# Optimization experiments

Hardware: AMD Instinct MI355X
Metric: run time of the kernel (lower is better)

## Reference

```python
import jax, jax.numpy as jnp
import numpy as np

D = 1024        # d_model
H = 16          # query heads
HKV = 4         # kv heads (GQA)
HD = D // H     # head dim = 64
MAX_T = 1024
EPS = 1e-6
CAP = 50.0      # logit softcap


def _rope_cache(max_t, hd):
    inv = 1.0 / (10000.0 ** (np.arange(0, hd, 2, dtype=np.float32) / hd))  # (hd/2,)
    t = np.arange(max_t, dtype=np.float32)
    f = np.outer(t, inv)                                                   # (max_t, hd/2)
    return jnp.asarray(np.cos(f)), jnp.asarray(np.sin(f))


def setup_inputs() -> dict:
    key = jax.random.key(0)
    ks = jax.random.split(key, 5)
    x = jax.random.normal(ks[0], (2, 64, 256, D), jnp.float32)  # (B,T,S,D)
    wq = jax.random.normal(ks[1], (D, H * HD), jnp.float32) * 0.02
    wk = jax.random.normal(ks[2], (D, HKV * HD), jnp.float32) * 0.02
    wv = jax.random.normal(ks[3], (D, HKV * HD), jnp.float32) * 0.02
    wo = jax.random.normal(ks[4], (H * HD, D), jnp.float32) * 0.02
    q_scale = jnp.ones((HD,), jnp.float32)  # QKNorm learnable gains
    k_scale = jnp.ones((HD,), jnp.float32)
    rope_cos, rope_sin = _rope_cache(MAX_T, HD)
    return {"x": x, "wq": wq, "wk": wk, "wv": wv, "wo": wo,
            "q_scale": q_scale, "k_scale": k_scale,
            "rope_cos": rope_cos, "rope_sin": rope_sin}


def _rmsnorm(v, scale):
    return v * jax.lax.rsqrt(jnp.mean(v * v, axis=-1, keepdims=True) + EPS) * scale


def reference(x, wq, wk, wv, wo, q_scale, k_scale, rope_cos, rope_sin):
    B, T, S, Dm = x.shape
    # fold spatial positions into batch: each position attends causally over time
    xt = x.transpose(0, 2, 1, 3).reshape(B * S, T, Dm)          # (N,T,D)
    q = (xt @ wq).reshape(B * S, T, H, HD)
    k = (xt @ wk).reshape(B * S, T, HKV, HD)
    v = (xt @ wv).reshape(B * S, T, HKV, HD)
    # QK-norm (RMSNorm over head_dim) before RoPE
    q = _rmsnorm(q, q_scale)
    k = _rmsnorm(k, k_scale)
    # 1D RoPE over temporal positions (split-half convention)
    cos = rope_cos[:T][None, :, None, :]                        # (1,T,1,HD/2)
    sin = rope_sin[:T][None, :, None, :]

    def rot(u):
        u1, u2 = jnp.split(u, 2, axis=-1)
        return jnp.concatenate([u1 * cos - u2 * sin, u1 * sin + u2 * cos], axis=-1)

    q = rot(q)
    k = rot(k)
    # GQA: expand kv heads to match query heads
    rep = H // HKV
    k = jnp.repeat(k, rep, axis=2)
    v = jnp.repeat(v, rep, axis=2)
    scores = jnp.einsum('nthd,nshd->nhts', q, k) / np.float32(np.sqrt(HD))
    scores = CAP * jnp.tanh(scores / CAP)                        # logit softcap
    causal = jnp.tril(jnp.ones((T, T), bool))
    scores = jnp.where(causal, scores, jnp.float32(-1e30))
    a = jax.nn.softmax(scores, axis=-1)
    o = jnp.einsum('nhts,nshd->nthd', a, v).reshape(B * S, T, H * HD) @ wo
    return o.reshape(B, S, T, Dm).transpose(0, 2, 1, 3)          # (B,T,S,D)
```

## Files before the change

kernel.cpp:

```cpp
#include <hip/hip_runtime.h>

#define DM   1024
#define NHQ  16
#define NKVH 4
#define HDIM 64
#define TTT  64
#define SSS  256
#define NBB  2
#define MROWS 32768
#define NQKV 1536

using short8 = __attribute__((ext_vector_type(8))) short;
using f32x4  = __attribute__((ext_vector_type(4))) float;

__device__ __forceinline__ short f2bf(float f) {
  union { float f; unsigned u; } v; v.f = f;
  unsigned r = v.u + 0x7fffu + ((v.u >> 16) & 1u);
  return (short)(r >> 16);
}

__device__ __forceinline__ f32x4 mfma16(short8 a, short8 b, f32x4 c) {
  return __builtin_amdgcn_mfma_f32_16x16x32_bf16(a, b, c, 0, 0, 0);
}

__device__ __forceinline__ void gload_lds16(const void* g, void* l) {
  __builtin_amdgcn_global_load_lds(
      (const __attribute__((address_space(1))) void*)g,
      (__attribute__((address_space(3))) void*)l, 16, 0, 0);
}

__global__ __launch_bounds__(256) void k_xconv(const float* __restrict__ x,
                                               short* __restrict__ xb) {
  int r = blockIdx.x;
  int n = r >> 6, t = r & 63;
  int b = n >> 8, s = n & 255;
  const float4* src = (const float4*)(x + ((size_t)((b * TTT + t) * SSS + s)) * DM);
  short4* dst = (short4*)(xb + (size_t)r * DM);
  float4 v = src[threadIdx.x];
  short4 o;
  o.x = f2bf(v.x); o.y = f2bf(v.y); o.z = f2bf(v.z); o.w = f2bf(v.w);
  dst[threadIdx.x] = o;
}

__global__ __launch_bounds__(256) void k_wt(const float* __restrict__ w,
                                            short* __restrict__ wt, int cols) {
  __shared__ float tile[32][33];
  int ctiles = cols >> 5;
  int tj = blockIdx.x % ctiles;
  int td = blockIdx.x / ctiles;
  int lx = threadIdx.x & 31, ly = threadIdx.x >> 5;
  #pragma unroll
  for (int rr = 0; rr < 32; rr += 8)
    tile[rr + ly][lx] = w[(size_t)(td * 32 + rr + ly) * cols + tj * 32 + lx];
  __syncthreads();
  #pragma unroll
  for (int rr = 0; rr < 32; rr += 8)
    wt[(size_t)(tj * 32 + rr + ly) * 1024 + td * 32 + lx] = f2bf(tile[lx][rr + ly]);
}

__device__ __forceinline__ void gemm_k1024(const short* __restrict__ Ab,
                                           const short* __restrict__ Bb,
                                           short* As, short* Bs,
                                           int tid, int lane, int wr, int wc,
                                           f32x4 (&acc)[4][4]) {
  const int ln15 = lane & 15, lhi = lane >> 4;
  for (int kt = 0; kt < 1024; kt += 64) {
    #pragma unroll
    for (int i = 0; i < 4; ++i) {
      int c = i * 256 + tid;
      int row = c >> 3, c8 = c & 7;
      gload_lds16(Ab + (size_t)row * 1024 + kt + c8 * 8, As + c * 8);
      gload_lds16(Bb + (size_t)row * 1024 + kt + c8 * 8, Bs + c * 8);
    }
    __syncthreads();
    #pragma unroll
    for (int kk = 0; kk < 2; ++kk) {
      int ko = kk * 32 + lhi * 8;
      short8 a[4], b[4];
      #pragma unroll
      for (int m = 0; m < 4; ++m)
        a[m] = *(const short8*)(As + (wr * 64 + m * 16 + ln15) * 64 + ko);
      #pragma unroll
      for (int n = 0; n < 4; ++n)
        b[n] = *(const short8*)(Bs + (wc * 64 + n * 16 + ln15) * 64 + ko);
      #pragma unroll
      for (int m = 0; m < 4; ++m)
        #pragma unroll
        for (int n = 0; n < 4; ++n)
          acc[m][n] = mfma16(a[m], b[n], acc[m][n]);
    }
    __syncthreads();
  }
}

__global__ __launch_bounds__(256) void k_qkv(
    const short* __restrict__ xb, const short* __restrict__ wt,
    const float* __restrict__ qscale, const float* __restrict__ kscale,
    const float* __restrict__ rcos, const float* __restrict__ rsin,
    short* __restrict__ qb, short* __restrict__ kb, short* __restrict__ vb) {
  __shared__ __align__(16) short As[128 * 64];
  __shared__ __align__(16) short Bs[128 * 64];
  int tn = blockIdx.x % 12, tm = blockIdx.x / 12;
  int tid = threadIdx.x, lane = tid & 63, wid = tid >> 6;
  int wr = wid >> 1, wc = wid & 1;
  f32x4 acc[4][4] = {};
  gemm_k1024(xb + (size_t)tm * 128 * 1024, wt + (size_t)tn * 128 * 1024,
             As, Bs, tid, lane, wr, wc, acc);
  int ln15 = lane & 15, lhi = lane >> 4;
  int j0 = tn * 128 + wc * 64;
  int r0 = tm * 128 + wr * 64;
  if (j0 < 1280) {
    const float* scale = (j0 < 1024) ? qscale : kscale;
    float sc[4];
    #pragma unroll
    for (int n = 0; n < 4; ++n) sc[n] = scale[n * 16 + ln15];
    #pragma unroll
    for (int m = 0; m < 4; ++m) {
      #pragma unroll
      for (int j = 0; j < 4; ++j) {
        float ss = 0.f;
        #pragma unroll
        for (int n = 0; n < 4; ++n) { float v = acc[m][n][j]; ss += v * v; }
        #pragma unroll
        for (int off = 8; off; off >>= 1) ss += __shfl_xor(ss, off, 64);
        float rms = rsqrtf(ss * (1.f / 64.f) + 1e-6f);
        int r = r0 + m * 16 + lhi * 4 + j;
        int t = r & 63;
        #pragma unroll
        for (int n = 0; n < 2; ++n) {
          int i = n * 16 + ln15;
          float cs = rcos[t * 32 + i], sn = rsin[t * 32 + i];
          float v1 = acc[m][n][j] * rms * sc[n];
          float v2 = acc[m][n + 2][j] * rms * sc[n + 2];
          float o1 = v1 * cs - v2 * sn;
          float o2 = v1 * sn + v2 * cs;
          if (j0 < 1024) {
            qb[(size_t)r * 1024 + j0 + i]      = f2bf(o1);
            qb[(size_t)r * 1024 + j0 + i + 32] = f2bf(o2);
          } else {
            int jk = j0 - 1024;
            kb[(size_t)r * 256 + jk + i]      = f2bf(o1);
            kb[(size_t)r * 256 + jk + i + 32] = f2bf(o2);
          }
        }
      }
    }
  } else {
    int jv = j0 - 1280;
    #pragma unroll
    for (int m = 0; m < 4; ++m)
      #pragma unroll
      for (int n = 0; n < 4; ++n)
        #pragma unroll
        for (int j = 0; j < 4; ++j) {
          int r = r0 + m * 16 + lhi * 4 + j;
          vb[(size_t)r * 256 + jv + n * 16 + ln15] = f2bf(acc[m][n][j]);
        }
  }
}

__global__ __launch_bounds__(256) void k_attn(const short* __restrict__ qb,
                                              const short* __restrict__ kb,
                                              const short* __restrict__ vb,
                                              short* __restrict__ ob) {
  __shared__ __align__(16) short Qs[64 * 72];
  __shared__ __align__(16) short Ks[64 * 72];
  __shared__ __align__(16) short Vt[64 * 72];
  __shared__ __align__(16) short Ps[64 * 72];
  int h = blockIdx.x & 15, n = blockIdx.x >> 4;
  int kvh = h >> 2;
  int tid = threadIdx.x, lane = tid & 63, wid = tid >> 6;
  for (int c = tid; c < 512; c += 256) {
    int row = c >> 3, c8 = c & 7;
    *(uint4*)(&Qs[row * 72 + c8 * 8]) =
        *(const uint4*)(qb + (size_t)(n * 64 + row) * 1024 + h * 64 + c8 * 8);
    *(uint4*)(&Ks[row * 72 + c8 * 8]) =
        *(const uint4*)(kb + (size_t)(n * 64 + row) * 256 + kvh * 64 + c8 * 8);
    short8 vv = *(const short8*)(vb + (size_t)(n * 64 + row) * 256 + kvh * 64 + c8 * 8);
    #pragma unroll
    for (int e = 0; e < 8; ++e) Vt[(c8 * 8 + e) * 72 + row] = vv[e];
  }
  __syncthreads();
  int ln15 = lane & 15, lhi = lane >> 4;
  f32x4 accs[4] = {};
  #pragma unroll
  for (int kk = 0; kk < 2; ++kk) {
    int ko = kk * 32 + lhi * 8;
    short8 aq = *(const short8*)(&Qs[(wid * 16 + ln15) * 72 + ko]);
    #pragma unroll
    for (int nn = 0; nn < 4; ++nn) {
      short8 bk = *(const short8*)(&Ks[(nn * 16 + ln15) * 72 + ko]);
      accs[nn] = mfma16(aq, bk, accs[nn]);
    }
  }
  int rowloc = wid * 16 + lhi * 4;
  float p[4][4];
  #pragma unroll
  for (int j = 0; j < 4; ++j) {
    int row = rowloc + j;
    float m = -3e38f;
    #pragma unroll
    for (int nn = 0; nn < 4; ++nn) {
      float s = accs[nn][j] * 0.125f;
      s = 50.f * tanhf(s * 0.02f);
      int col = nn * 16 + ln15;
      s = (col <= row) ? s : -1e30f;
      p[nn][j] = s;
      m = fmaxf(m, s);
    }
    #pragma unroll
    for (int off = 8; off; off >>= 1) m = fmaxf(m, __shfl_xor(m, off, 64));
    float sum = 0.f;
    #pragma unroll
    for (int nn = 0; nn < 4; ++nn) {
      float e = __expf(p[nn][j] - m);
      p[nn][j] = e; sum += e;
    }
    #pragma unroll
    for (int off = 8; off; off >>= 1) sum += __shfl_xor(sum, off, 64);
    float inv = 1.f / sum;
    #pragma unroll
    for (int nn = 0; nn < 4; ++nn) p[nn][j] *= inv;
  }
  #pragma unroll
  for (int nn = 0; nn < 4; ++nn)
    #pragma unroll
    for (int j = 0; j < 4; ++j)
      Ps[(rowloc + j) * 72 + nn * 16 + ln15] = f2bf(p[nn][j]);
  __syncthreads();
  f32x4 acco[4] = {};
  #pragma unroll
  for (int kk = 0; kk < 2; ++kk) {
    int ko = kk * 32 + lhi * 8;
    short8 ap = *(const short8*)(&Ps[(wid * 16 + ln15) * 72 + ko]);
    #pragma unroll
    for (int nn = 0; nn < 4; ++nn) {
      short8 bv = *(const short8*)(&Vt[(nn * 16 + ln15) * 72 + ko]);
      acco[nn] = mfma16(ap, bv, acco[nn]);
    }
  }
  #pragma unroll
  for (int nn = 0; nn < 4; ++nn)
    #pragma unroll
    for (int j = 0; j < 4; ++j) {
      int t = rowloc + j;
      ob[(size_t)(n * 64 + t) * 1024 + h * 64 + nn * 16 + ln15] = f2bf(acco[nn][j]);
    }
}

__global__ __launch_bounds__(256) void k_out(const short* __restrict__ ab,
                                             const short* __restrict__ wt,
                                             float* __restrict__ out) {
  __shared__ __align__(16) short As[128 * 64];
  __shared__ __align__(16) short Bs[128 * 64];
  int tn = blockIdx.x & 7, tm = blockIdx.x >> 3;
  int tid = threadIdx.x, lane = tid & 63, wid = tid >> 6;
  int wr = wid >> 1, wc = wid & 1;
  f32x4 acc[4][4] = {};
  gemm_k1024(ab + (size_t)tm * 128 * 1024, wt + (size_t)tn * 128 * 1024,
             As, Bs, tid, lane, wr, wc, acc);
  int ln15 = lane & 15, lhi = lane >> 4;
  #pragma unroll
  for (int m = 0; m < 4; ++m)
    #pragma unroll
    for (int j = 0; j < 4; ++j) {
      int r = tm * 128 + wr * 64 + m * 16 + lhi * 4 + j;
      int nseq = r >> 6, t = r & 63;
      int b = nseq >> 8, s = nseq & 255;
      float* orow = out + ((size_t)((b * TTT + t) * SSS + s)) * DM + tn * 128 + wc * 64;
      #pragma unroll
      for (int n = 0; n < 4; ++n)
        orow[n * 16 + ln15] = acc[m][n][j];
    }
}

extern "C" void kernel_launch(void* const* d_in, const int* in_sizes, int n_in,
                              void* d_out, int out_size, void* d_ws, size_t ws_size,
                              hipStream_t stream) {
  const float* x  = (const float*)d_in[0];
  const float* wq = (const float*)d_in[1];
  const float* wk = (const float*)d_in[2];
  const float* wv = (const float*)d_in[3];
  const float* wo = (const float*)d_in[4];
  const float* qs = (const float*)d_in[5];
  const float* ks = (const float*)d_in[6];
  const float* rc = (const float*)d_in[7];
  const float* rs = (const float*)d_in[8];
  float* out = (float*)d_out;
  char* ws = (char*)d_ws;

  short* xb    = (short*)(ws);
  short* wqkvT = (short*)(ws + 67108864);
  short* woT   = (short*)(ws + 70254592);
  short* qb    = (short*)(ws + 72351744);
  short* kb    = (short*)(ws + 139460608);
  short* vb    = (short*)(ws + 156237824);
  short* ob    = xb;

  k_xconv<<<MROWS, 256, 0, stream>>>(x, xb);
  k_wt<<<1024, 256, 0, stream>>>(wq, wqkvT, 1024);
  k_wt<<<256, 256, 0, stream>>>(wk, wqkvT + (size_t)1024 * 1024, 256);
  k_wt<<<256, 256, 0, stream>>>(wv, wqkvT + (size_t)1280 * 1024, 256);
  k_wt<<<1024, 256, 0, stream>>>(wo, woT, 1024);
  k_qkv<<<256 * 12, 256, 0, stream>>>(xb, wqkvT, qs, ks, rc, rs, qb, kb, vb);
  k_attn<<<512 * 16, 256, 0, stream>>>(qb, kb, vb, ob);
  k_out<<<256 * 8, 256, 0, stream>>>(ob, woT, out);
}
```

Measured before the change: 382.5 us.

## Use 256x256 double-buffered GEMM tiles with swizzled grid and LDS-staged epilogue stores

Both GEMM kernels move from 128x128 tiles with 256 threads to 256x256 tiles with 512 threads. Each wave now accumulates 128x64, and global-to-LDS loads are double-buffered so the next K-slab loads while MFMAs run on the current one. The block index is swizzled to improve L2 reuse of A/B panels. Epilogues stage results in LDS and write rows with wide 16-byte stores instead of scattered 2- or 4-byte stores. The cost is 128KB of LDS per block and more accumulator registers, so only one block fits per CU and the grid has fewer blocks, which risks tail imbalance.

```diff
diff --git a/kernel.cpp b/kernel.cpp
--- a/kernel.cpp
+++ b/kernel.cpp
@@ -8,7 +8,6 @@
 #define SSS  256
 #define NBB  2
 #define MROWS 32768
-#define NQKV 1536
 
 using short8 = __attribute__((ext_vector_type(8))) short;
 using f32x4  = __attribute__((ext_vector_type(4))) float;
@@ -58,64 +57,72 @@
     wt[(size_t)(tj * 32 + rr + ly) * 1024 + td * 32 + lx] = f2bf(tile[lx][rr + ly]);
 }
 
-__device__ __forceinline__ void gemm_k1024(const short* __restrict__ Ab,
-                                           const short* __restrict__ Bb,
-                                           short* As, short* Bs,
-                                           int tid, int lane, int wr, int wc,
-                                           f32x4 (&acc)[4][4]) {
-  const int ln15 = lane & 15, lhi = lane >> 4;
-  for (int kt = 0; kt < 1024; kt += 64) {
-    #pragma unroll
-    for (int i = 0; i < 4; ++i) {
-      int c = i * 256 + tid;
-      int row = c >> 3, c8 = c & 7;
-      gload_lds16(Ab + (size_t)row * 1024 + kt + c8 * 8, As + c * 8);
-      gload_lds16(Bb + (size_t)row * 1024 + kt + c8 * 8, Bs + c * 8);
-    }
-    __syncthreads();
-    #pragma unroll
-    for (int kk = 0; kk < 2; ++kk) {
-      int ko = kk * 32 + lhi * 8;
-      short8 a[4], b[4];
-      #pragma unroll
-      for (int m = 0; m < 4; ++m)
-        a[m] = *(const short8*)(As + (wr * 64 + m * 16 + ln15) * 64 + ko);
-      #pragma unroll
-      for (int n = 0; n < 4; ++n)
-        b[n] = *(const short8*)(Bs + (wc * 64 + n * 16 + ln15) * 64 + ko);
-      #pragma unroll
-      for (int m = 0; m < 4; ++m)
-        #pragma unroll
-        for (int n = 0; n < 4; ++n)
-          acc[m][n] = mfma16(a[m], b[n], acc[m][n]);
-    }
-    __syncthreads();
-  }
-}
-
-__global__ __launch_bounds__(256) void k_qkv(
+#define GEMM256_BODY(Ab, Bb)                                                   \
+  const int tid = threadIdx.x, lane = tid & 63, wid = tid >> 6;                \
+  const int wr = wid >> 2, wc = wid & 3;                                       \
+  const int ln15 = lane & 15, lhi = lane >> 4;                                 \
+  f32x4 acc[8][4] = {};                                                        \
+  auto STAGE = [&](short* dA, short* dB, int kt) {                             \
+    _Pragma("unroll")                                                          \
+    for (int rr = 0; rr < 4; ++rr) {                                           \
+      int c = rr * 512 + tid;                                                  \
+      int row = c >> 3, c8 = c & 7;                                            \
+      gload_lds16(Ab + (size_t)row * 1024 + kt + c8 * 8, dA + c * 8);          \
+      gload_lds16(Bb + (size_t)row * 1024 + kt + c8 * 8, dB + c * 8);          \
+    }                                                                          \
+  };                                                                           \
+  auto COMPUTE = [&](const short* cA, const short* cB) {                       \
+    _Pragma("unroll")                                                          \
+    for (int kk = 0; kk < 2; ++kk) {                                           \
+      const int ko = kk * 32 + lhi * 8;                                        \
+      short8 a[8], b[4];                                                       \
+      _Pragma("unroll")                                                        \
+      for (int n = 0; n < 4; ++n)                                              \
+        b[n] = *(const short8*)(cB + (wc * 64 + n * 16 + ln15) * 64 + ko);     \
+      _Pragma("unroll")                                                        \
+      for (int m = 0; m < 8; ++m)                                              \
+        a[m] = *(const short8*)(cA + (wr * 128 + m * 16 + ln15) * 64 + ko);    \
+      _Pragma("unroll")                                                        \
+      for (int m = 0; m < 8; ++m)                                              \
+        _Pragma("unroll")                                                      \
+        for (int n = 0; n < 4; ++n) acc[m][n] = mfma16(a[m], b[n], acc[m][n]); \
+    }                                                                          \
+  };                                                                           \
+  STAGE(sm, sm + 16384, 0);                                                    \
+  __syncthreads();                                                             \
+  for (int t = 0; t < 15; ++t) {                                               \
+    short* cA = (t & 1) ? sm + 32768 : sm;                                     \
+    short* cB = (t & 1) ? sm + 49152 : sm + 16384;                             \
+    short* nA = (t & 1) ? sm : sm + 32768;                                     \
+    short* nB = (t & 1) ? sm + 16384 : sm + 49152;                             \
+    STAGE(nA, nB, (t + 1) * 64);                                               \
+    COMPUTE(cA, cB);                                                           \
+    __syncthreads();                                                           \
+  }                                                                            \
+  COMPUTE(sm + 32768, sm + 49152);                                             \
+  __syncthreads();
+
+__global__ __launch_bounds__(512) void k_qkv(
     const short* __restrict__ xb, const short* __restrict__ wt,
     const float* __restrict__ qscale, const float* __restrict__ kscale,
     const float* __restrict__ rcos, const float* __restrict__ rsin,
     short* __restrict__ qb, short* __restrict__ kb, short* __restrict__ vb) {
-  __shared__ __align__(16) short As[128 * 64];
-  __shared__ __align__(16) short Bs[128 * 64];
-  int tn = blockIdx.x % 12, tm = blockIdx.x / 12;
-  int tid = threadIdx.x, lane = tid & 63, wid = tid >> 6;
-  int wr = wid >> 1, wc = wid & 1;
-  f32x4 acc[4][4] = {};
-  gemm_k1024(xb + (size_t)tm * 128 * 1024, wt + (size_t)tn * 128 * 1024,
-             As, Bs, tid, lane, wr, wc, acc);
-  int ln15 = lane & 15, lhi = lane >> 4;
-  int j0 = tn * 128 + wc * 64;
-  int r0 = tm * 128 + wr * 64;
-  if (j0 < 1280) {
-    const float* scale = (j0 < 1024) ? qscale : kscale;
+  __shared__ __align__(16) short sm[65536];
+  const int bid = blockIdx.x;
+  const int swz = (bid & 7) * 96 + (bid >> 3);
+  const int tn = swz % 6, tm = swz / 6;
+  const short* Ab = xb + (size_t)tm * 256 * 1024;
+  const short* Bb = wt + (size_t)tn * 256 * 1024;
+  GEMM256_BODY(Ab, Bb)
+
+  short* ot = sm;
+  if (tn < 5) {
+    const float* scale = (tn < 4) ? qscale : kscale;
     float sc[4];
     #pragma unroll
     for (int n = 0; n < 4; ++n) sc[n] = scale[n * 16 + ln15];
     #pragma unroll
-    for (int m = 0; m < 4; ++m) {
+    for (int m = 0; m < 8; ++m) {
       #pragma unroll
       for (int j = 0; j < 4; ++j) {
         float ss = 0.f;
@@ -124,38 +131,42 @@
         #pragma unroll
         for (int off = 8; off; off >>= 1) ss += __shfl_xor(ss, off, 64);
         float rms = rsqrtf(ss * (1.f / 64.f) + 1e-6f);
-        int r = r0 + m * 16 + lhi * 4 + j;
-        int t = r & 63;
+        int rl = wr * 128 + m * 16 + lhi * 4 + j;
+        int t = (tm * 256 + rl) & 63;
         #pragma unroll
         for (int n = 0; n < 2; ++n) {
           int i = n * 16 + ln15;
           float cs = rcos[t * 32 + i], sn = rsin[t * 32 + i];
           float v1 = acc[m][n][j] * rms * sc[n];
           float v2 = acc[m][n + 2][j] * rms * sc[n + 2];
-          float o1 = v1 * cs - v2 * sn;
-          float o2 = v1 * sn + v2 * cs;
-          if (j0 < 1024) {
-            qb[(size_t)r * 1024 + j0 + i]      = f2bf(o1);
-            qb[(size_t)r * 1024 + j0 + i + 32] = f2bf(o2);
-          } else {
-            int jk = j0 - 1024;
-            kb[(size_t)r * 256 + jk + i]      = f2bf(o1);
-            kb[(size_t)r * 256 + jk + i + 32] = f2bf(o2);
-          }
+          ot[rl * 256 + wc * 64 + i]      = f2bf(v1 * cs - v2 * sn);
+          ot[rl * 256 + wc * 64 + i + 32] = f2bf(v1 * sn + v2 * cs);
         }
       }
     }
   } else {
-    int jv = j0 - 1280;
-    #pragma unroll
-    for (int m = 0; m < 4; ++m)
+    #pragma unroll
+    for (int m = 0; m < 8; ++m)
       #pragma unroll
       for (int n = 0; n < 4; ++n)
         #pragma unroll
         for (int j = 0; j < 4; ++j) {
-          int r = r0 + m * 16 + lhi * 4 + j;
-          vb[(size_t)r * 256 + jv + n * 16 + ln15] = f2bf(acc[m][n][j]);
+          int rl = wr * 128 + m * 16 + lhi * 4 + j;
+          ot[rl * 256 + wc * 64 + n * 16 + ln15] = f2bf(acc[m][n][j]);
         }
+  }
+  __syncthreads();
+  {
+    int row = tid >> 1, half = tid & 1;
+    int r = tm * 256 + row;
+    const uint4* src = (const uint4*)(ot + row * 256 + half * 128);
+    short* dst;
+    if (tn < 4)       dst = qb + (size_t)r * 1024 + tn * 256 + half * 128;
+    else if (tn == 4) dst = kb + (size_t)r * 256 + half * 128;
+    else              dst = vb + (size_t)r * 256 + half * 128;
+    uint4* d4 = (uint4*)dst;
+    #pragma unroll
+    for (int i = 0; i < 16; ++i) d4[i] = src[i];
   }
 }
 
@@ -248,30 +259,43 @@
     }
 }
 
-__global__ __launch_bounds__(256) void k_out(const short* __restrict__ ab,
+__global__ __launch_bounds__(512) void k_out(const short* __restrict__ ab,
                                              const short* __restrict__ wt,
                                              float* __restrict__ out) {
-  __shared__ __align__(16) short As[128 * 64];
-  __shared__ __align__(16) short Bs[128 * 64];
-  int tn = blockIdx.x & 7, tm = blockIdx.x >> 3;
-  int tid = threadIdx.x, lane = tid & 63, wid = tid >> 6;
-  int wr = wid >> 1, wc = wid & 1;
-  f32x4 acc[4][4] = {};
-  gemm_k1024(ab + (size_t)tm * 128 * 1024, wt + (size_t)tn * 128 * 1024,
-             As, Bs, tid, lane, wr, wc, acc);
-  int ln15 = lane & 15, lhi = lane >> 4;
-  #pragma unroll
-  for (int m = 0; m < 4; ++m)
-    #pragma unroll
-    for (int j = 0; j < 4; ++j) {
-      int r = tm * 128 + wr * 64 + m * 16 + lhi * 4 + j;
+  __shared__ __align__(16) short sm[65536];
+  const int bid = blockIdx.x;
+  const int swz = (bid & 7) * 64 + (bid >> 3);
+  const int tn = swz & 3, tm = swz >> 2;
+  const short* Ab = ab + (size_t)tm * 256 * 1024;
+  const short* Bb = wt + (size_t)tn * 256 * 1024;
+  GEMM256_BODY(Ab, Bb)
+
+  float* of = (float*)sm;
+  #pragma unroll
+  for (int ch = 0; ch < 2; ++ch) {
+    if (wr == ch) {
+      #pragma unroll
+      for (int m = 0; m < 8; ++m)
+        #pragma unroll
+        for (int n = 0; n < 4; ++n)
+          #pragma unroll
+          for (int j = 0; j < 4; ++j)
+            of[(m * 16 + lhi * 4 + j) * 256 + wc * 64 + n * 16 + ln15] = acc[m][n][j];
+    }
+    __syncthreads();
+    {
+      int row = tid >> 2, q4 = tid & 3;
+      int r = tm * 256 + ch * 128 + row;
       int nseq = r >> 6, t = r & 63;
       int b = nseq >> 8, s = nseq & 255;
-      float* orow = out + ((size_t)((b * TTT + t) * SSS + s)) * DM + tn * 128 + wc * 64;
+      float* dst = out + ((size_t)((b * TTT + t) * SSS + s)) * DM + tn * 256 + q4 * 64;
+      const float4* src = (const float4*)(of + row * 256 + q4 * 64);
+      float4* d4 = (float4*)dst;
       #pragma unroll
-      for (int n = 0; n < 4; ++n)
-        orow[n * 16 + ln15] = acc[m][n][j];
-    }
+      for (int i = 0; i < 16; ++i) d4[i] = src[i];
+    }
+    __syncthreads();
+  }
 }
 
 extern "C" void kernel_launch(void* const* d_in, const int* in_sizes, int n_in,
@@ -302,7 +326,7 @@
   k_wt<<<256, 256, 0, stream>>>(wk, wqkvT + (size_t)1024 * 1024, 256);
   k_wt<<<256, 256, 0, stream>>>(wv, wqkvT + (size_t)1280 * 1024, 256);
   k_wt<<<1024, 256, 0, stream>>>(wo, woT, 1024);
-  k_qkv<<<256 * 12, 256, 0, stream>>>(xb, wqkvT, qs, ks, rc, rs, qb, kb, vb);
+  k_qkv<<<768, 512, 0, stream>>>(xb, wqkvT, qs, ks, rc, rs, qb, kb, vb);
   k_attn<<<512 * 16, 256, 0, stream>>>(qb, kb, vb, ob);
-  k_out<<<256 * 8, 256, 0, stream>>>(ob, woT, out);
-}
+  k_out<<<512, 512, 0, stream>>>(ob, woT, out);
+}
```

New measurement: 354.5 us. 7.3% less time.
